# Optimization experiments

Hardware: AMD Instinct MI355X
Metric: run time of the kernel (lower is better)

## Reference

```python
import jax, jax.numpy as jnp
import numpy as np
from jax import lax

BIG = 1e10  # initial distance, matching torch's 1e10


def farthest_point_sample(xyz, init_farthest, npoint):
    """xyz: [B,N,3] float; init_farthest: [B] int32; returns centroids [B,npoint] int32."""
    B, N, _ = xyz.shape
    batch_idx = jnp.arange(B)

    def body(i, state):
        centroids, distance, farthest = state
        centroids = centroids.at[:, i].set(farthest)
        c = xyz[batch_idx, farthest][:, None, :]              # [B,1,3] current centroid
        dist = jnp.sum(jnp.square(xyz - c), axis=-1)          # [B,N] sq. distance
        distance = jnp.minimum(distance, dist)                # mask-update: keep min dist to any centroid
        farthest = jnp.argmax(distance, axis=-1).astype(jnp.int32)
        return centroids, distance, farthest

    centroids0 = jnp.zeros((B, npoint), jnp.int32)
    distance0 = jnp.full((B, N), BIG, xyz.dtype)
    centroids, _, _ = lax.fori_loop(0, npoint, body, (centroids0, distance0, init_farthest.astype(jnp.int32)))
    return centroids


def setup_inputs() -> dict:
    key = jax.random.key(0)
    k1, k2, k3 = jax.random.split(key, 3)
    B, N = 16, 100000
    mesh = jax.random.normal(k1, (B, N, 3), dtype=jnp.float32)
    contact_map = jax.random.uniform(k2, (B, N, 1), dtype=jnp.float32)
    init_farthest = jax.random.randint(k3, (B,), 0, N, dtype=jnp.int32)
    return {"mesh": mesh, "contact_map": contact_map, "init_farthest": init_farthest, "npoint": 1024}


def reference(mesh, contact_map, init_farthest, npoint):
    B, N, _ = mesh.shape
    batch_idx = jnp.arange(B)

    # __compute_mesh_scale: max distance from centroid, per batch
    centroid = jnp.mean(mesh, axis=1, keepdims=True)                      # [B,1,3]
    s_obj = jnp.max(jnp.sqrt(jnp.sum(jnp.square(mesh - centroid), axis=2)), axis=1)  # [B]

    # __farthest_point_sample
    centroids = farthest_point_sample(mesh, init_farthest, npoint)        # [B,npoint]

    # gather sampled points and contact values
    point_cloud = mesh[batch_idx[:, None], centroids]                     # [B,npoint,3]
    cm_sampled = contact_map[batch_idx[:, None], centroids]               # [B,npoint,1]

    # normalize by object scale (broadcast over points/coords)
    point_cloud_norm = point_cloud / s_obj[:, None, None]

    # point_cloud_norm_contact fed to the contact encoder in the original
    return jnp.concatenate([cm_sampled, point_cloud_norm], axis=2)        # [B,npoint,4]
```

## Files before the change

kernel.cpp:

```cpp
#include <hip/hip_runtime.h>
#include <cstdint>

#define NBATCH 16
#define NPTS   100000
#define NPOINT 1024
#define GPB    16
#define TPB    256
#define WPB    4
#define NSUB   16
#define STRIDE (GPB * TPB)
#define KPT    25
#define NPAIR  13

typedef unsigned long long u64;


__global__ __launch_bounds__(256) void sum_kernel(const float* __restrict__ xyz,
                                                  float* __restrict__ psum) {
    const int b   = blockIdx.x & 15;
    const int sub = blockIdx.x >> 4;
    const float* P = xyz + (size_t)b * NPTS * 3;
    float sx = 0.f, sy = 0.f, sz = 0.f;
    for (int i = sub * TPB + threadIdx.x; i < NPTS; i += NSUB * TPB) {
        sx += P[i * 3 + 0];
        sy += P[i * 3 + 1];
        sz += P[i * 3 + 2];
    }
    #pragma unroll
    for (int off = 32; off; off >>= 1) {
        sx += __shfl_xor(sx, off);
        sy += __shfl_xor(sy, off);
        sz += __shfl_xor(sz, off);
    }
    __shared__ float r[3][4];
    const int wave = threadIdx.x >> 6, lane = threadIdx.x & 63;
    if (lane == 0) { r[0][wave] = sx; r[1][wave] = sy; r[2][wave] = sz; }
    __syncthreads();
    if (threadIdx.x == 0) {
        float* o = psum + (b * NSUB + sub) * 4;
        o[0] = r[0][0] + r[0][1] + r[0][2] + r[0][3];
        o[1] = r[1][0] + r[1][1] + r[1][2] + r[1][3];
        o[2] = r[2][0] + r[2][1] + r[2][2] + r[2][3];
    }
}

__global__ __launch_bounds__(256) void max_kernel(const float* __restrict__ xyz,
                                                  const float* __restrict__ psum,
                                                  unsigned* __restrict__ pmax,
                                                  u64* __restrict__ slots) {
    if (blockIdx.x == 0) {
        slots[threadIdx.x] = 0ull;
        slots[threadIdx.x + 256] = 0ull;
    }
    const int b   = blockIdx.x & 15;
    const int sub = blockIdx.x >> 4;
    const float* P = xyz + (size_t)b * NPTS * 3;
    float sx = 0.f, sy = 0.f, sz = 0.f;
    #pragma unroll
    for (int s = 0; s < NSUB; ++s) {
        sx += psum[(b * NSUB + s) * 4 + 0];
        sy += psum[(b * NSUB + s) * 4 + 1];
        sz += psum[(b * NSUB + s) * 4 + 2];
    }
    const float mx = sx / (float)NPTS, my = sy / (float)NPTS, mz = sz / (float)NPTS;
    float best = 0.f;
    for (int i = sub * TPB + threadIdx.x; i < NPTS; i += NSUB * TPB) {
        float dx = P[i * 3 + 0] - mx;
        float dy = P[i * 3 + 1] - my;
        float dz = P[i * 3 + 2] - mz;
        best = fmaxf(best, dx * dx + dy * dy + dz * dz);
    }
    #pragma unroll
    for (int off = 32; off; off >>= 1) best = fmaxf(best, __shfl_xor(best, off));
    __shared__ float r[4];
    const int wave = threadIdx.x >> 6, lane = threadIdx.x & 63;
    if (lane == 0) r[wave] = best;
    __syncthreads();
    if (threadIdx.x == 0)
        pmax[b * NSUB + sub] = __float_as_uint(fmaxf(fmaxf(r[0], r[1]), fmaxf(r[2], r[3])));
}

__global__ __launch_bounds__(256, 1) void fps_kernel(const float* __restrict__ xyz,
                                                     const float* __restrict__ cmap,
                                                     const int* __restrict__ init_far,
                                                     const unsigned* __restrict__ pmax,
                                                     u64* __restrict__ slots,
                                                     float* __restrict__ out) {
    const int b   = blockIdx.x & 15;
    const int g   = blockIdx.x >> 4;
    const int tid = threadIdx.x;
    const int wave = tid >> 6, lane = tid & 63;
    const int tl  = g * TPB + tid;
    const float* P = xyz + (size_t)b * NPTS * 3;

    float m = 0.f;
    #pragma unroll
    for (int s = 0; s < NSUB; ++s) m = fmaxf(m, __uint_as_float(pmax[b * NSUB + s]));
    const float sb = sqrtf(m);

    float pxx[NPAIR], pxy[NPAIR], pyx[NPAIR], pyy[NPAIR],
          pzx[NPAIR], pzy[NPAIR], pdx[NPAIR], pdy[NPAIR];
    #pragma unroll
    for (int j = 0; j < NPAIR; ++j) {
        const int p0 = tl + (2 * j) * STRIDE;
        const int p1 = tl + (2 * j + 1) * STRIDE;
        const bool v0 = p0 < NPTS, v1 = p1 < NPTS;
        pxx[j] = v0 ? P[p0 * 3 + 0] : 0.f;  pxy[j] = v1 ? P[p1 * 3 + 0] : 0.f;
        pyx[j] = v0 ? P[p0 * 3 + 1] : 0.f;  pyy[j] = v1 ? P[p1 * 3 + 1] : 0.f;
        pzx[j] = v0 ? P[p0 * 3 + 2] : 0.f;  pzy[j] = v1 ? P[p1 * 3 + 2] : 0.f;
        pdx[j] = v0 ? 1e10f : -1.0f;        pdy[j] = v1 ? 1e10f : -1.0f;
    }

    __shared__ u64 lds_key[WPB];
    __shared__ int lds_win;

    int cur = init_far[b];
    float cx = P[cur * 3 + 0], cy = P[cur * 3 + 1], cz = P[cur * 3 + 2];
    const bool wrblk = (g == 0);

    for (int i = 0; i < NPOINT; ++i) {
        if (i == NPOINT - 1) {
            if (wrblk && tid == 64) {
                float* o = out + ((size_t)b * NPOINT + i) * 4;
                o[0] = cmap[(size_t)b * NPTS + cur];
                o[1] = cx / sb; o[2] = cy / sb; o[3] = cz / sb;
            }
            break;
        }

        float best = -1.0f;
        int bidx = 0;
        {
            #pragma clang fp contract(off)
            #pragma unroll
            for (int j = 0; j < NPAIR; ++j) {
                float dx0 = pxx[j] - cx, dx1 = pxy[j] - cx;
                float dy0 = pyx[j] - cy, dy1 = pyy[j] - cy;
                float dz0 = pzx[j] - cz, dz1 = pzy[j] - cz;
                float s0 = dx0 * dx0 + dy0 * dy0;  float s1 = dx1 * dx1 + dy1 * dy1;
                s0 = s0 + dz0 * dz0;               s1 = s1 + dz1 * dz1;
                float n0 = fminf(pdx[j], s0);      float n1 = fminf(pdy[j], s1);
                pdx[j] = n0;                       pdy[j] = n1;
                if (n0 > best) { best = n0; bidx = tl + (2 * j) * STRIDE; }
                if (n1 > best) { best = n1; bidx = tl + (2 * j + 1) * STRIDE; }
            }
        }

        const u64 want = (u64)(i + 1);
        u64 key = ((u64)__float_as_uint(best) << 22) | (u64)(0x3FFFFFu - (unsigned)bidx);
        #pragma unroll
        for (int off = 32; off; off >>= 1) {
            u64 o2 = __shfl_xor(key, off);
            key = o2 > key ? o2 : key;
        }
        if (lane == 0) lds_key[wave] = key;
        __syncthreads();

        u64* const bs = slots + ((size_t)(i & 1) * NBATCH + b) * GPB;

        if (wave == 0) {
            u64 bk = (lane < WPB) ? lds_key[lane] : 0;
            #pragma unroll
            for (int off = 1; off < WPB; off <<= 1) {
                u64 o2 = __shfl_xor(bk, off);
                bk = o2 > bk ? o2 : bk;
            }
            if (lane == 0)
                __hip_atomic_store(&bs[g], bk | (want << 54),
                                   __ATOMIC_RELAXED, __HIP_MEMORY_SCOPE_AGENT);

            u64 v = 0;
            if (lane < GPB) {
                u64* sp = &bs[lane];
                int tries = 0;
                for (;;) {
                    v = __hip_atomic_load(sp, __ATOMIC_RELAXED, __HIP_MEMORY_SCOPE_AGENT);
                    if ((v >> 54) >= want) break;
                    if (++tries > 16) __builtin_amdgcn_s_sleep(1);
                }
            }
            #pragma unroll
            for (int off = 8; off; off >>= 1) {
                u64 o2 = __shfl_xor(v, off);
                v = o2 > v ? o2 : v;
            }
            if (lane == 0)
                lds_win = (int)(0x3FFFFFu - (unsigned)(v & 0x3FFFFFu));
        } else if (wave == 1 && wrblk && lane == 0) {
            float* o = out + ((size_t)b * NPOINT + i) * 4;
            o[0] = cmap[(size_t)b * NPTS + cur];
            o[1] = cx / sb; o[2] = cy / sb; o[3] = cz / sb;
        }
        __syncthreads();
        cur = lds_win;
        cx = P[cur * 3 + 0];
        cy = P[cur * 3 + 1];
        cz = P[cur * 3 + 2];
    }
}

extern "C" void kernel_launch(void* const* d_in, const int* in_sizes, int n_in,
                              void* d_out, int out_size, void* d_ws, size_t ws_size,
                              hipStream_t stream) {
    const float* mesh = (const float*)d_in[0];
    const float* cmap = (const float*)d_in[1];
    const int* init   = (const int*)d_in[2];
    float* out = (float*)d_out;

    char* ws      = (char*)d_ws;
    float* psum   = (float*)ws;
    unsigned* pmx = (unsigned*)(ws + 4096);
    u64* slots    = (u64*)(ws + 8192);

    sum_kernel<<<dim3(256), dim3(TPB), 0, stream>>>(mesh, psum);
    max_kernel<<<dim3(256), dim3(TPB), 0, stream>>>(mesh, psum, pmx, slots);
    fps_kernel<<<dim3(256), dim3(TPB), 0, stream>>>(mesh, cmap, init, pmx, slots, out);
}
```

Before: 2.004 ms.

## Carry winner coordinates through cross-block slots to skip dependent global reload

Each block now records the coordinates of its local farthest point and publishes them with the key through four per-block slots. Each slot word carries the iteration tag, so a reader only accepts a complete message, and the winning coordinates come straight from the slots instead of a dependent global load of the winner's xyz each iteration. The wave-level argmax reduces a 32-bit distance and uses ballot for ties, replacing a 64-bit key shuffle. In exchange each message is wider, polling uses inline-asm quad loads with cache bypass, and the slot workspace is four times larger.

New measurement: 3.175 ms. +58.4%, slower.

```diff
diff --git a/kernel.cpp b/kernel.cpp
--- a/kernel.cpp
+++ b/kernel.cpp
@@ -2,8 +2,8 @@
 #include <cstdint>
 
 #define NBATCH 16
+#define NPOINT 1024
 #define NPTS   100000
-#define NPOINT 1024
 #define GPB    16
 #define TPB    256
 #define WPB    4
@@ -14,6 +14,17 @@
 
 typedef unsigned long long u64;
 
+
+__device__ __forceinline__ void quad_load(const u64* p, u64& a, u64& b, u64& c, u64& d) {
+    asm volatile(
+        "global_load_dwordx2 %0, %4, off sc0 sc1\n\t"
+        "global_load_dwordx2 %1, %4, off offset:8 sc0 sc1\n\t"
+        "global_load_dwordx2 %2, %4, off offset:16 sc0 sc1\n\t"
+        "global_load_dwordx2 %3, %4, off offset:24 sc0 sc1\n\t"
+        "s_waitcnt vmcnt(0)"
+        : "=&v"(a), "=&v"(b), "=&v"(c), "=&v"(d)
+        : "v"(p) : "memory");
+}
 
 __global__ __launch_bounds__(256) void sum_kernel(const float* __restrict__ xyz,
                                                   float* __restrict__ psum) {
@@ -49,8 +60,8 @@
                                                   unsigned* __restrict__ pmax,
                                                   u64* __restrict__ slots) {
     if (blockIdx.x == 0) {
-        slots[threadIdx.x] = 0ull;
-        slots[threadIdx.x + 256] = 0ull;
+        #pragma unroll
+        for (int q = 0; q < 8; ++q) slots[threadIdx.x + q * 256] = 0ull;
     }
     const int b   = blockIdx.x & 15;
     const int sub = blockIdx.x >> 4;
@@ -93,10 +104,10 @@
     const int tl  = g * TPB + tid;
     const float* P = xyz + (size_t)b * NPTS * 3;
 
-    float m = 0.f;
-    #pragma unroll
-    for (int s = 0; s < NSUB; ++s) m = fmaxf(m, __uint_as_float(pmax[b * NSUB + s]));
-    const float sb = sqrtf(m);
+    float m0 = 0.f;
+    #pragma unroll
+    for (int s = 0; s < NSUB; ++s) m0 = fmaxf(m0, __uint_as_float(pmax[b * NSUB + s]));
+    const float sb = sqrtf(m0);
 
     float pxx[NPAIR], pxy[NPAIR], pyx[NPAIR], pyy[NPAIR],
           pzx[NPAIR], pzy[NPAIR], pdx[NPAIR], pdy[NPAIR];
@@ -111,8 +122,10 @@
         pdx[j] = v0 ? 1e10f : -1.0f;        pdy[j] = v1 ? 1e10f : -1.0f;
     }
 
-    __shared__ u64 lds_key[WPB];
-    __shared__ int lds_win;
+    __shared__ u64   lkey[WPB];
+    __shared__ float lx[WPB], ly[WPB], lz[WPB];
+    __shared__ float bcx_s, bcy_s, bcz_s;
+    __shared__ int   bcur_s;
 
     int cur = init_far[b];
     float cx = P[cur * 3 + 0], cy = P[cur * 3 + 1], cz = P[cur * 3 + 2];
@@ -128,7 +141,7 @@
             break;
         }
 
-        float best = -1.0f;
+        float best = -1.0f, bx = 0.f, by = 0.f, bz = 0.f;
         int bidx = 0;
         {
             #pragma clang fp contract(off)
@@ -141,61 +154,92 @@
                 s0 = s0 + dz0 * dz0;               s1 = s1 + dz1 * dz1;
                 float n0 = fminf(pdx[j], s0);      float n1 = fminf(pdy[j], s1);
                 pdx[j] = n0;                       pdy[j] = n1;
-                if (n0 > best) { best = n0; bidx = tl + (2 * j) * STRIDE; }
-                if (n1 > best) { best = n1; bidx = tl + (2 * j + 1) * STRIDE; }
-            }
-        }
-
-        const u64 want = (u64)(i + 1);
-        u64 key = ((u64)__float_as_uint(best) << 22) | (u64)(0x3FFFFFu - (unsigned)bidx);
+                if (n0 > best) { best = n0; bidx = tl + (2*j)   * STRIDE;
+                                 bx = pxx[j]; by = pyx[j]; bz = pzx[j]; }
+                if (n1 > best) { best = n1; bidx = tl + (2*j+1) * STRIDE;
+                                 bx = pxy[j]; by = pyy[j]; bz = pzy[j]; }
+            }
+        }
+
+        const unsigned db = __float_as_uint(best);
+        unsigned wm = db;
         #pragma unroll
         for (int off = 32; off; off >>= 1) {
-            u64 o2 = __shfl_xor(key, off);
-            key = o2 > key ? o2 : key;
-        }
-        if (lane == 0) lds_key[wave] = key;
+            unsigned o2 = __shfl_xor(wm, off);
+            wm = o2 > wm ? o2 : wm;
+        }
+        const u64 mask = __ballot(db == wm);
+        bool amwin;
+        if (__popcll(mask) == 1) {
+            amwin = (lane == __ffsll(mask) - 1);
+        } else {
+            int mine = (db == wm) ? bidx : 0x7FFFFFFF;
+            #pragma unroll
+            for (int off = 32; off; off >>= 1) mine = min(mine, __shfl_xor(mine, off));
+            amwin = (db == wm) && (bidx == mine);
+        }
+        if (amwin) {
+            lkey[wave] = ((u64)wm << 22) | (u64)(0x3FFFFFu - (unsigned)bidx);
+            lx[wave] = bx; ly[wave] = by; lz[wave] = bz;
+        }
         __syncthreads();
 
-        u64* const bs = slots + ((size_t)(i & 1) * NBATCH + b) * GPB;
+        const u64 want = (u64)(i + 1);
+        const unsigned want32 = (unsigned)want;
+        u64* const bs = slots + ((size_t)(i & 1) * NBATCH + b) * (GPB * 4);
 
         if (wave == 0) {
-            u64 bk = (lane < WPB) ? lds_key[lane] : 0;
+            u64 k4 = (lane < WPB) ? lkey[lane] : 0;
+            u64 bk = k4;
             #pragma unroll
             for (int off = 1; off < WPB; off <<= 1) {
                 u64 o2 = __shfl_xor(bk, off);
                 bk = o2 > bk ? o2 : bk;
             }
-            if (lane == 0)
-                __hip_atomic_store(&bs[g], bk | (want << 54),
+            const int wv = __ffsll(__ballot((lane < WPB) && (k4 == bk))) - 1;
+
+            u64 msg = 0;
+            if      (lane == 0) msg = bk | (want << 54);
+            else if (lane == 1) msg = (u64)__float_as_uint(lx[wv]) | (want << 32);
+            else if (lane == 2) msg = (u64)__float_as_uint(ly[wv]) | (want << 32);
+            else if (lane == 3) msg = (u64)__float_as_uint(lz[wv]) | (want << 32);
+            if (lane < 4)
+                __hip_atomic_store(&bs[g * 4 + lane], msg,
                                    __ATOMIC_RELAXED, __HIP_MEMORY_SCOPE_AGENT);
 
-            u64 v = 0;
+            u64 w0 = 0, w1 = 0, w2 = 0, w3 = 0;
             if (lane < GPB) {
-                u64* sp = &bs[lane];
+                const u64* sp = &bs[lane * 4];
                 int tries = 0;
                 for (;;) {
-                    v = __hip_atomic_load(sp, __ATOMIC_RELAXED, __HIP_MEMORY_SCOPE_AGENT);
-                    if ((v >> 54) >= want) break;
+                    quad_load(sp, w0, w1, w2, w3);
+                    if ((w0 >> 54) >= want &&
+                        (unsigned)(w1 >> 32) == want32 &&
+                        (unsigned)(w2 >> 32) == want32 &&
+                        (unsigned)(w3 >> 32) == want32) break;
                     if (++tries > 16) __builtin_amdgcn_s_sleep(1);
                 }
             }
-            #pragma unroll
-            for (int off = 8; off; off >>= 1) {
-                u64 o2 = __shfl_xor(v, off);
-                v = o2 > v ? o2 : v;
-            }
-            if (lane == 0)
-                lds_win = (int)(0x3FFFFFu - (unsigned)(v & 0x3FFFFFu));
+            u64 kk = w0;
+            #pragma unroll
+            for (int off = 1; off < GPB; off <<= 1) {
+                u64 o2 = __shfl_xor(kk, off);
+                kk = o2 > kk ? o2 : kk;
+            }
+            if (lane < GPB && w0 == kk) {
+                bcur_s = (int)(0x3FFFFFu - (unsigned)(kk & 0x3FFFFFu));
+                bcx_s = __uint_as_float((unsigned)w1);
+                bcy_s = __uint_as_float((unsigned)w2);
+                bcz_s = __uint_as_float((unsigned)w3);
+            }
         } else if (wave == 1 && wrblk && lane == 0) {
             float* o = out + ((size_t)b * NPOINT + i) * 4;
             o[0] = cmap[(size_t)b * NPTS + cur];
             o[1] = cx / sb; o[2] = cy / sb; o[3] = cz / sb;
         }
         __syncthreads();
-        cur = lds_win;
-        cx = P[cur * 3 + 0];
-        cy = P[cur * 3 + 1];
-        cz = P[cur * 3 + 2];
+        cur = bcur_s;
+        cx = bcx_s; cy = bcy_s; cz = bcz_s;
     }
 }
 
```
